# Kernel optimization log

Hardware: AMD Instinct MI355X
Metric: run time of the kernel (lower is better)

## Reference

```python
import jax, jax.numpy as jnp
import numpy as np

K = 16  # K_neighbors

def linear_positions(pixels):
    # normalized flat (pixels, 2) grid positions, matching LinearPositions(normalize=True, flat_output=True)
    wd = int(round(pixels ** 0.5))
    h = jnp.repeat(jnp.arange(wd, dtype=jnp.float32)[:, None], wd, axis=1)
    w = jnp.repeat(jnp.arange(wd, dtype=jnp.float32)[None, :], wd, axis=0)
    pos = jnp.stack([h, w], axis=-1) / (wd - 1)
    return pos.reshape(pixels, 2)


def setup_inputs() -> dict:
    key = jax.random.key(0)
    ks = jax.random.split(key, 8)
    B, Wn, P, C = 4, 16, 256, 32
    inp = {
        "x": jax.random.normal(ks[0], (B, Wn, P, C), dtype=jnp.float32),
        "sf_w0": jax.random.normal(ks[1], (3 * K, 128), dtype=jnp.float32) * 0.05,
        "sf_b0": jnp.zeros((128,), jnp.float32),
        "sf_w1": jax.random.normal(ks[2], (128, 128), dtype=jnp.float32) * 0.05,
        "sf_b1": jnp.zeros((128,), jnp.float32),
        "sf_wo": jax.random.normal(ks[3], (128, 64), dtype=jnp.float32) * 0.05,
        "sf_bo": jnp.zeros((64,), jnp.float32),
        "out_w0": jax.random.normal(ks[4], (C + 64, 128), dtype=jnp.float32) * 0.05,
        "out_b0": jnp.zeros((128,), jnp.float32),
        "out_w1": jax.random.normal(ks[5], (128, 128), dtype=jnp.float32) * 0.05,
        "out_b1": jnp.zeros((128,), jnp.float32),
        "out_wo": jax.random.normal(ks[6], (128, 64), dtype=jnp.float32) * 0.05,
        "out_bo": jnp.zeros((64,), jnp.float32),
    }
    return inp


def reference(x, sf_w0, sf_b0, sf_w1, sf_b1, sf_wo, sf_bo,
              out_w0, out_b0, out_w1, out_b1, out_wo, out_bo):
    B, Wn, P, C = x.shape
    # L1 similarity: 1 - mean |x_i - x_j| over channels -> (B, Wn, P, P)
    w = 1.0 - jnp.mean(jnp.abs(x[:, :, :, None, :] - x[:, :, None, :, :]), axis=-1)
    K_scores, K_idxs = jax.lax.top_k(w, K)  # (B, Wn, P, K)
    pos = linear_positions(P)  # (P, 2)
    # source pos for pixel i minus gathered target pos of its K neighbors
    rel = pos[None, None, :, None, :] - pos[K_idxs]  # (B, Wn, P, K, 2)
    K_rel_pos = rel.reshape(B, Wn, P, K * 2)
    # sf FFN
    h = jnp.concatenate([K_scores, K_rel_pos], axis=-1)  # (B, Wn, P, 3K)
    h = jax.nn.relu(h @ sf_w0 + sf_b0)
    h = jax.nn.relu(h @ sf_w1 + sf_b1)
    sf = h @ sf_wo + sf_bo  # (B, Wn, P, 64)
    # out FFN
    h = jnp.concatenate([x, sf], axis=-1)  # (B, Wn, P, C+64)
    h = jax.nn.relu(h @ out_w0 + out_b0)
    h = jax.nn.relu(h @ out_w1 + out_b1)
    return h @ out_wo + out_bo  # (B, Wn, P, 64)
```

## Files before the change

### kernel.cpp

```cpp
#include <hip/hip_runtime.h>
#include <hip/hip_bf16.h>

#define K_SEL 16
#define NCAND 20

typedef __attribute__((ext_vector_type(8))) short short8;
typedef __attribute__((ext_vector_type(4))) short short4v;
typedef __attribute__((ext_vector_type(4))) float f32x4;

__device__ __forceinline__ short f2bf_bits(float v) {
    union { __hip_bfloat16 b; short s; } u;
    u.b = __float2bfloat16(v);
    return u.s;
}
__device__ __forceinline__ float bf2f_bits(short h) {
    return __uint_as_float(((unsigned)(unsigned short)h) << 16);
}
__device__ __forceinline__ float readlane_f(float v, int l) {
    return __int_as_float(__builtin_amdgcn_readlane(__float_as_int(v), l));
}

__device__ __noinline__ void pack_body(
    int t,
    const float* __restrict__ s0w, const float* __restrict__ s1w,
    const float* __restrict__ sow, const float* __restrict__ o0w,
    const float* __restrict__ o1w, const float* __restrict__ oow,
    short* __restrict__ wpack)
{
    if (t >= 69632) return;
    int l, base;
    if      (t <  8192) { l = 0; base = 0;     }
    else if (t < 24576) { l = 1; base = 8192;  }
    else if (t < 32768) { l = 2; base = 24576; }
    else if (t < 45056) { l = 3; base = 32768; }
    else if (t < 61440) { l = 4; base = 45056; }
    else                { l = 5; base = 61440; }

    const float* W = (l == 0) ? s0w : (l == 1) ? s1w : (l == 2) ? sow
                   : (l == 3) ? o0w : (l == 4) ? o1w : oow;
    int N    = (l == 2 || l == 5) ? 64 : 128;
    int Kr   = (l == 0) ? 48 : (l == 3) ? 96 : 128;
    int woff = (l == 0) ? 0 : (l == 1) ? 16384 : (l == 2) ? 49152
             : (l == 3) ? 65536 : (l == 4) ? 90112 : 122880;
    int sz   = (l == 2 || l == 5) ? 8192 : (l == 3) ? 12288 : (l == 0) ? 8192 : 16384;

    int e = t - base;
    int i = e & 7, kb = (e >> 3) & 3, rem = e >> 5;
    int n = rem % N, ks = rem / N;
    int k = ks * 32 + kb * 8 + i;
    float v = (k < Kr) ? W[k * N + n] : 0.0f;
    short hi = f2bf_bits(v);
    float lo = v - bf2f_bits(hi);
    wpack[woff + e]      = hi;
    wpack[woff + sz + e] = f2bf_bits(lo);
}

template<int COMP>
__device__ __forceinline__ void simtopk_body(
    const float* __restrict__ x, float* __restrict__ feat,
    float* xsT, int* candj, double* rs, int win, int grp, int tid)
{
    const int lane = tid & 63;
    const int wv   = tid >> 6;

    if (tid < 512) {
        const int c4 = tid & 7, jb = tid >> 3;
        const float4* gx = reinterpret_cast<const float4*>(x + (size_t)win * 8192);
        float4 v0 = gx[jb * 8 + c4];
        float4 v1 = gx[jb * 8 + c4 + 512];
        float4 v2 = gx[jb * 8 + c4 + 1024];
        float4 v3 = gx[jb * 8 + c4 + 1536];
        float4* xsT4 = reinterpret_cast<float4*>(xsT);
        const int gsw = jb ^ c4;
        xsT4[(4 * c4 + 0) * 64 + gsw] = make_float4(v0.x, v1.x, v2.x, v3.x);
        xsT4[(4 * c4 + 1) * 64 + gsw] = make_float4(v0.y, v1.y, v2.y, v3.y);
        xsT4[(4 * c4 + 2) * 64 + gsw] = make_float4(v0.z, v1.z, v2.z, v3.z);
        xsT4[(4 * c4 + 3) * 64 + gsw] = make_float4(v0.w, v1.w, v2.w, v3.w);
    }
    __syncthreads();

    const int plbase = (grp & 1) * 32 + wv * 2;

    const f32x4* xsT4c = reinterpret_cast<const f32x4*>(xsT);
    float acc0[4] = {0.f, 0.f, 0.f, 0.f};
    float acc1[4] = {0.f, 0.f, 0.f, 0.f};
    #pragma unroll
    for (int c = 0; c < 32; ++c) {
        f32x4 a = xsT4c[c * 64 + (lane ^ ((c >> 2) & 7))];
        float xi0 = readlane_f(a[COMP], plbase);
        float xi1 = readlane_f(a[COMP], plbase + 1);
        #pragma unroll
        for (int q = 0; q < 4; ++q) {
            acc0[q] += fabsf(a[q] - xi0);
            acc1[q] += fabsf(a[q] - xi1);
        }
    }
    unsigned int p0[4], p1[4];
    #pragma unroll
    for (int q = 0; q < 4; ++q) {
        p0[q] = (__float_as_uint(acc0[q]) & 0xFFFFFF00u) | (unsigned)(q * 64 + lane);
        p1[q] = (__float_as_uint(acc1[q]) & 0xFFFFFF00u) | (unsigned)(q * 64 + lane);
    }

    unsigned int T0 = 0, T1 = 0;
    for (int bit = 31; bit >= 0; --bit) {
        unsigned int c0 = T0 | (1u << bit), c1 = T1 | (1u << bit);
        int n0 = __popcll(__ballot(p0[0] < c0)) + __popcll(__ballot(p0[1] < c0))
               + __popcll(__ballot(p0[2] < c0)) + __popcll(__ballot(p0[3] < c0));
        int n1 = __popcll(__ballot(p1[0] < c1)) + __popcll(__ballot(p1[1] < c1))
               + __popcll(__ballot(p1[2] < c1)) + __popcll(__ballot(p1[3] < c1));
        if (n0 < NCAND) T0 = c0;
        if (n1 < NCAND) T1 = c1;
    }

    const unsigned long long lt = (1ull << lane) - 1ull;
    int base0 = 0, base1 = 0;
    #pragma unroll
    for (int q = 0; q < 4; ++q) {
        bool s0 = (p0[q] <= T0);
        unsigned long long m0 = __ballot(s0);
        if (s0) candj[(wv * 2 + 0) * NCAND + base0 + __popcll(m0 & lt)] = q * 64 + lane;
        base0 += __popcll(m0);
        bool s1 = (p1[q] <= T1);
        unsigned long long m1 = __ballot(s1);
        if (s1) candj[(wv * 2 + 1) * NCAND + base1 + __popcll(m1 & lt)] = q * 64 + lane;
        base1 += __popcll(m1);
    }
    asm volatile("s_waitcnt lgkmcnt(0)" ::: "memory");

    const int t  = lane >> 5;
    const int cl = lane & 31;
    double s = 0.0;
    int myj = -1;
    if (cl < NCAND) {
        myj = candj[(wv * 2 + t) * NCAND + cl];
        const int pwin = COMP * 64 + plbase + t;
        const float4* xj = reinterpret_cast<const float4*>(x + (size_t)win * 8192 + (size_t)myj * 32);
        const float4* xp = reinterpret_cast<const float4*>(x + (size_t)win * 8192 + (size_t)pwin * 32);
        #pragma unroll
        for (int c4 = 0; c4 < 8; ++c4) {
            float4 b = xj[c4];
            float4 a = xp[c4];
            s += fabs((double)a.x - (double)b.x);
            s += fabs((double)a.y - (double)b.y);
            s += fabs((double)a.z - (double)b.z);
            s += fabs((double)a.w - (double)b.w);
        }
        rs[(wv * 2 + t) * NCAND + cl] = s;
    }
    asm volatile("s_waitcnt lgkmcnt(0)" ::: "memory");

    if (cl < NCAND) {
        int rank = 0;
        #pragma unroll 4
        for (int o = 0; o < NCAND; ++o) {
            double so = rs[(wv * 2 + t) * NCAND + o];
            int    jo = candj[(wv * 2 + t) * NCAND + o];
            rank += (so < s || (so == s && jo < myj)) ? 1 : 0;
        }
        if (rank < K_SEL) {
            const int pwin = COMP * 64 + plbase + t;
            const int gp   = win * 256 + pwin;
            feat[gp * 48 + rank] = (float)(1.0 - s * 0.03125);
            float dh = (float)((pwin >> 4) - (myj >> 4)) * (1.0f / 15.0f);
            float dw = (float)((pwin & 15) - (myj & 15)) * (1.0f / 15.0f);
            reinterpret_cast<float2*>(feat)[gp * 24 + 8 + rank] = make_float2(dh, dw);
        }
    }
}

__global__ __launch_bounds__(1024) void simtopk_kernel(
    const float* __restrict__ x,
    float* __restrict__ feat,
    const float* __restrict__ s0w, const float* __restrict__ s1w,
    const float* __restrict__ sow, const float* __restrict__ o0w,
    const float* __restrict__ o1w, const float* __restrict__ oow,
    short* __restrict__ wpack)
{
    __shared__ __align__(16) float xsT[8192];
    __shared__ int    candj[16 * 2 * NCAND];
    __shared__ double rs[16 * 2 * NCAND];

    const int tid = threadIdx.x;

    if (blockIdx.x >= 512) {
        pack_body((blockIdx.x - 512) * 1024 + tid,
                  s0w, s1w, sow, o0w, o1w, oow, wpack);
        return;
    }

    const int win = blockIdx.x >> 3;
    const int grp = blockIdx.x & 7;

    switch (grp >> 1) {
        case 0: simtopk_body<0>(x, feat, xsT, candj, rs, win, grp, tid); break;
        case 1: simtopk_body<1>(x, feat, xsT, candj, rs, win, grp, tid); break;
        case 2: simtopk_body<2>(x, feat, xsT, candj, rs, win, grp, tid); break;
        default: simtopk_body<3>(x, feat, xsT, candj, rs, win, grp, tid); break;
    }
}

template<int K_STEPS, int N, bool RELU, bool TO_GLOBAL>
__device__ __forceinline__ void bf16_layer(
    const short* hiIn, const short* loIn, short* hiOut, short* loOut,
    float* gout, int pbase, const short* __restrict__ wpack, int woff, int sz,
    const float* __restrict__ bias, int wv, int lane, int out_col_off)
{
    if (N == 64 && wv >= 8) return;
    const int mt  = wv & 1;
    const int nt  = wv >> 1;
    const int m_a = mt * 16 + (lane & 15);
    const int kb  = lane >> 4;
    const int n   = nt * 16 + (lane & 15);

    f32x4 acc = (f32x4){0.f, 0.f, 0.f, 0.f};
    #pragma unroll
    for (int ks = 0; ks < K_STEPS; ++ks) {
        const int g   = ks * 4 + kb;
        const int off = m_a * 256 + ((g ^ (m_a & 7)) << 4);
        short8 ahi = *(const short8*)((const char*)hiIn + off);
        short8 alo = *(const short8*)((const char*)loIn + off);
        const int wi = woff + ((ks * N + n) * 4 + kb) * 8;
        short8 whi = *(const short8*)(wpack + wi);
        short8 wlo = *(const short8*)(wpack + wi + sz);
        acc = __builtin_amdgcn_mfma_f32_16x16x32_bf16(ahi, whi, acc, 0, 0, 0);
        acc = __builtin_amdgcn_mfma_f32_16x16x32_bf16(ahi, wlo, acc, 0, 0, 0);
        acc = __builtin_amdgcn_mfma_f32_16x16x32_bf16(alo, whi, acc, 0, 0, 0);
    }

    const float bv = bias[n];
    #pragma unroll
    for (int r = 0; r < 4; ++r) {
        float v = acc[r] + bv;
        if (RELU) v = fmaxf(v, 0.0f);
        const int pw = mt * 16 + (lane >> 4) * 4 + r;
        if (TO_GLOBAL) {
            gout[(size_t)(pbase + pw) * 64 + n] = v;
        } else {
            const int w   = out_col_off + n;
            const int off = pw * 256 + ((((w >> 3) ^ (pw & 7))) << 4) + (w & 7) * 2;
            short h = f2bf_bits(v);
            short l = f2bf_bits(v - bf2f_bits(h));
            *(short*)((char*)hiOut + off) = h;
            *(short*)((char*)loOut + off) = l;
        }
    }
}

__global__ __launch_bounds__(1024) void ffn_kernel(
    const float* __restrict__ x,
    const float* __restrict__ feat,
    const short* __restrict__ wpack,
    const float* __restrict__ s0b, const float* __restrict__ s1b,
    const float* __restrict__ sob, const float* __restrict__ o0b,
    const float* __restrict__ o1b, const float* __restrict__ oob,
    float* __restrict__ out)
{
    __shared__ __align__(16) short hiA[32 * 128];
    __shared__ __align__(16) short loA[32 * 128];
    __shared__ __align__(16) short hiB[32 * 128];
    __shared__ __align__(16) short loB[32 * 128];

    const int tid   = threadIdx.x;
    const int lane  = tid & 63;
    const int wv    = tid >> 6;
    const int pbase = blockIdx.x * 32;

    if (tid < 384) {
        int p = tid / 12, c4 = tid - p * 12;
        f32x4 v = ((const f32x4*)feat)[(size_t)(pbase + p) * 12 + c4];
        short4v h4, l4;
        #pragma unroll
        for (int j = 0; j < 4; ++j) {
            short h = f2bf_bits(v[j]);
            h4[j] = h;
            l4[j] = f2bf_bits(v[j] - bf2f_bits(h));
        }
        int off = p * 256 + ((((c4 >> 1) ^ (p & 7))) << 4) + (c4 & 1) * 8;
        *(short4v*)((char*)hiA + off) = h4;
        *(short4v*)((char*)loA + off) = l4;
    } else if (tid < 512) {
        int t2 = tid - 384;
        int p = t2 & 31, sel = t2 >> 5;
        int g = 6 + (sel & 1);
        int off = p * 256 + ((g ^ (p & 7)) << 4);
        short8 z = (short8){0,0,0,0,0,0,0,0};
        if (sel >> 1) *(short8*)((char*)loA + off) = z;
        else          *(short8*)((char*)hiA + off) = z;
    }
    __syncthreads();

    bf16_layer<2, 128, true, false>(hiA, loA, hiB, loB, nullptr, pbase,
                                    wpack, 0, 8192, s0b, wv, lane, 0);
    __syncthreads();
    bf16_layer<4, 128, true, false>(hiB, loB, hiA, loA, nullptr, pbase,
                                    wpack, 16384, 16384, s1b, wv, lane, 0);
    __syncthreads();
    if (tid < 256) {
        int p = tid >> 3, c4 = tid & 7;
        f32x4 v = ((const f32x4*)x)[(size_t)(pbase + p) * 8 + c4];
        short4v h4, l4;
        #pragma unroll
        for (int j = 0; j < 4; ++j) {
            short h = f2bf_bits(v[j]);
            h4[j] = h;
            l4[j] = f2bf_bits(v[j] - bf2f_bits(h));
        }
        int off = p * 256 + ((((c4 >> 1) ^ (p & 7))) << 4) + (c4 & 1) * 8;
        *(short4v*)((char*)hiB + off) = h4;
        *(short4v*)((char*)loB + off) = l4;
    }
    bf16_layer<4, 64, false, false>(hiA, loA, hiB, loB, nullptr, pbase,
                                    wpack, 49152, 8192, sob, wv, lane, 32);
    __syncthreads();
    bf16_layer<3, 128, true, false>(hiB, loB, hiA, loA, nullptr, pbase,
                                    wpack, 65536, 12288, o0b, wv, lane, 0);
    __syncthreads();
    bf16_layer<4, 128, true, false>(hiA, loA, hiB, loB, nullptr, pbase,
                                    wpack, 90112, 16384, o1b, wv, lane, 0);
    __syncthreads();
    bf16_layer<4, 64, false, true>(hiB, loB, nullptr, nullptr, out, pbase,
                                   wpack, 122880, 8192, oob, wv, lane, 0);
}

extern "C" void kernel_launch(void* const* d_in, const int* in_sizes, int n_in,
                              void* d_out, int out_size, void* d_ws, size_t ws_size,
                              hipStream_t stream) {
    const float* x    = (const float*)d_in[0];
    const float* s0w  = (const float*)d_in[1];
    const float* s0b  = (const float*)d_in[2];
    const float* s1w  = (const float*)d_in[3];
    const float* s1b  = (const float*)d_in[4];
    const float* sow  = (const float*)d_in[5];
    const float* sob  = (const float*)d_in[6];
    const float* o0w  = (const float*)d_in[7];
    const float* o0b  = (const float*)d_in[8];
    const float* o1w  = (const float*)d_in[9];
    const float* o1b  = (const float*)d_in[10];
    const float* oow  = (const float*)d_in[11];
    const float* oob  = (const float*)d_in[12];

    short* wpack = (short*)d_ws;
    float* feat  = (float*)((char*)d_ws + 524288);
    float* out   = (float*)d_out;

    simtopk_kernel<<<580, 1024, 0, stream>>>(x, feat,
                                             s0w, s1w, sow, o0w, o1w, oow, wpack);
    ffn_kernel<<<512, 1024, 0, stream>>>(x, feat, wpack,
                                         s0b, s1b, sob, o0b, o1b, oob,
                                         out);
}
```

Baseline: 53.73 us.

## Process 64 pixels per FFN block with 8 waves reusing weight fragments across M tiles

The FFN kernel now handles 64 pixels per block with 512 threads instead of 32 pixels with 1024 threads. Each wave owns one N tile and loops over several M tiles, so each weight fragment loaded from global memory feeds up to four row tiles instead of one. This cuts global weight traffic per pixel and halves the block count. In exchange it doubles shared memory per block and raises register pressure from the multiple accumulators, and the grid shrinks to 256 blocks, which may leave compute units idle.

```diff
diff --git a/kernel.cpp b/kernel.cpp
--- a/kernel.cpp
+++ b/kernel.cpp
@@ -201,53 +201,62 @@
 }
 
 template<int K_STEPS, int N, bool RELU, bool TO_GLOBAL>
-__device__ __forceinline__ void bf16_layer(
+__device__ __forceinline__ void bf16_layer64(
     const short* hiIn, const short* loIn, short* hiOut, short* loOut,
     float* gout, int pbase, const short* __restrict__ wpack, int woff, int sz,
     const float* __restrict__ bias, int wv, int lane, int out_col_off)
 {
-    if (N == 64 && wv >= 8) return;
-    const int mt  = wv & 1;
-    const int nt  = wv >> 1;
-    const int m_a = mt * 16 + (lane & 15);
-    const int kb  = lane >> 4;
-    const int n   = nt * 16 + (lane & 15);
-
-    f32x4 acc = (f32x4){0.f, 0.f, 0.f, 0.f};
+    const int nt   = (N == 128) ? wv : (wv & 3);
+    const int mt0  = (N == 128) ? 0  : ((wv >> 2) * 2);
+    const int MREP = (N == 128) ? 4  : 2;
+    const int kb   = lane >> 4;
+    const int n    = nt * 16 + (lane & 15);
+
+    f32x4 acc[4];
+    #pragma unroll
+    for (int m = 0; m < 4; ++m) acc[m] = (f32x4){0.f, 0.f, 0.f, 0.f};
+
     #pragma unroll
     for (int ks = 0; ks < K_STEPS; ++ks) {
-        const int g   = ks * 4 + kb;
-        const int off = m_a * 256 + ((g ^ (m_a & 7)) << 4);
-        short8 ahi = *(const short8*)((const char*)hiIn + off);
-        short8 alo = *(const short8*)((const char*)loIn + off);
         const int wi = woff + ((ks * N + n) * 4 + kb) * 8;
         short8 whi = *(const short8*)(wpack + wi);
         short8 wlo = *(const short8*)(wpack + wi + sz);
-        acc = __builtin_amdgcn_mfma_f32_16x16x32_bf16(ahi, whi, acc, 0, 0, 0);
-        acc = __builtin_amdgcn_mfma_f32_16x16x32_bf16(ahi, wlo, acc, 0, 0, 0);
-        acc = __builtin_amdgcn_mfma_f32_16x16x32_bf16(alo, whi, acc, 0, 0, 0);
+        const int g = ks * 4 + kb;
+        #pragma unroll
+        for (int m = 0; m < MREP; ++m) {
+            const int m_a = (mt0 + m) * 16 + (lane & 15);
+            const int off = m_a * 256 + ((g ^ (m_a & 7)) << 4);
+            short8 ahi = *(const short8*)((const char*)hiIn + off);
+            short8 alo = *(const short8*)((const char*)loIn + off);
+            acc[m] = __builtin_amdgcn_mfma_f32_16x16x32_bf16(ahi, whi, acc[m], 0, 0, 0);
+            acc[m] = __builtin_amdgcn_mfma_f32_16x16x32_bf16(ahi, wlo, acc[m], 0, 0, 0);
+            acc[m] = __builtin_amdgcn_mfma_f32_16x16x32_bf16(alo, whi, acc[m], 0, 0, 0);
+        }
     }
 
     const float bv = bias[n];
     #pragma unroll
-    for (int r = 0; r < 4; ++r) {
-        float v = acc[r] + bv;
-        if (RELU) v = fmaxf(v, 0.0f);
-        const int pw = mt * 16 + (lane >> 4) * 4 + r;
-        if (TO_GLOBAL) {
-            gout[(size_t)(pbase + pw) * 64 + n] = v;
-        } else {
-            const int w   = out_col_off + n;
-            const int off = pw * 256 + ((((w >> 3) ^ (pw & 7))) << 4) + (w & 7) * 2;
-            short h = f2bf_bits(v);
-            short l = f2bf_bits(v - bf2f_bits(h));
-            *(short*)((char*)hiOut + off) = h;
-            *(short*)((char*)loOut + off) = l;
-        }
-    }
-}
-
-__global__ __launch_bounds__(1024) void ffn_kernel(
+    for (int m = 0; m < MREP; ++m) {
+        #pragma unroll
+        for (int r = 0; r < 4; ++r) {
+            float v = acc[m][r] + bv;
+            if (RELU) v = fmaxf(v, 0.0f);
+            const int pw = (mt0 + m) * 16 + (lane >> 4) * 4 + r;
+            if (TO_GLOBAL) {
+                gout[(size_t)(pbase + pw) * 64 + n] = v;
+            } else {
+                const int w   = out_col_off + n;
+                const int off = pw * 256 + ((((w >> 3) ^ (pw & 7))) << 4) + (w & 7) * 2;
+                short h = f2bf_bits(v);
+                short l = f2bf_bits(v - bf2f_bits(h));
+                *(short*)((char*)hiOut + off) = h;
+                *(short*)((char*)loOut + off) = l;
+            }
+        }
+    }
+}
+
+__global__ __launch_bounds__(512) void ffn_kernel(
     const float* __restrict__ x,
     const float* __restrict__ feat,
     const short* __restrict__ wpack,
@@ -256,32 +265,36 @@
     const float* __restrict__ o1b, const float* __restrict__ oob,
     float* __restrict__ out)
 {
-    __shared__ __align__(16) short hiA[32 * 128];
-    __shared__ __align__(16) short loA[32 * 128];
-    __shared__ __align__(16) short hiB[32 * 128];
-    __shared__ __align__(16) short loB[32 * 128];
+    __shared__ __align__(16) short hiA[64 * 128];
+    __shared__ __align__(16) short loA[64 * 128];
+    __shared__ __align__(16) short hiB[64 * 128];
+    __shared__ __align__(16) short loB[64 * 128];
 
     const int tid   = threadIdx.x;
     const int lane  = tid & 63;
     const int wv    = tid >> 6;
-    const int pbase = blockIdx.x * 32;
-
-    if (tid < 384) {
-        int p = tid / 12, c4 = tid - p * 12;
-        f32x4 v = ((const f32x4*)feat)[(size_t)(pbase + p) * 12 + c4];
-        short4v h4, l4;
-        #pragma unroll
-        for (int j = 0; j < 4; ++j) {
-            short h = f2bf_bits(v[j]);
-            h4[j] = h;
-            l4[j] = f2bf_bits(v[j] - bf2f_bits(h));
-        }
-        int off = p * 256 + ((((c4 >> 1) ^ (p & 7))) << 4) + (c4 & 1) * 8;
-        *(short4v*)((char*)hiA + off) = h4;
-        *(short4v*)((char*)loA + off) = l4;
-    } else if (tid < 512) {
-        int t2 = tid - 384;
-        int p = t2 & 31, sel = t2 >> 5;
+    const int pbase = blockIdx.x * 64;
+
+    #pragma unroll
+    for (int rr = 0; rr < 2; ++rr) {
+        int u = tid + rr * 512;
+        if (u < 768) {
+            int p = u / 12, c4 = u - p * 12;
+            f32x4 v = ((const f32x4*)feat)[(size_t)(pbase + p) * 12 + c4];
+            short4v h4, l4;
+            #pragma unroll
+            for (int j = 0; j < 4; ++j) {
+                short h = f2bf_bits(v[j]);
+                h4[j] = h;
+                l4[j] = f2bf_bits(v[j] - bf2f_bits(h));
+            }
+            int off = p * 256 + ((((c4 >> 1) ^ (p & 7))) << 4) + (c4 & 1) * 8;
+            *(short4v*)((char*)hiA + off) = h4;
+            *(short4v*)((char*)loA + off) = l4;
+        }
+    }
+    if (tid < 256) {
+        int p = tid >> 2, sel = tid & 3;
         int g = 6 + (sel & 1);
         int off = p * 256 + ((g ^ (p & 7)) << 4);
         short8 z = (short8){0,0,0,0,0,0,0,0};
@@ -290,13 +303,13 @@
     }
     __syncthreads();
 
-    bf16_layer<2, 128, true, false>(hiA, loA, hiB, loB, nullptr, pbase,
-                                    wpack, 0, 8192, s0b, wv, lane, 0);
-    __syncthreads();
-    bf16_layer<4, 128, true, false>(hiB, loB, hiA, loA, nullptr, pbase,
-                                    wpack, 16384, 16384, s1b, wv, lane, 0);
-    __syncthreads();
-    if (tid < 256) {
+    bf16_layer64<2, 128, true, false>(hiA, loA, hiB, loB, nullptr, pbase,
+                                      wpack, 0, 8192, s0b, wv, lane, 0);
+    __syncthreads();
+    bf16_layer64<4, 128, true, false>(hiB, loB, hiA, loA, nullptr, pbase,
+                                      wpack, 16384, 16384, s1b, wv, lane, 0);
+    __syncthreads();
+    {
         int p = tid >> 3, c4 = tid & 7;
         f32x4 v = ((const f32x4*)x)[(size_t)(pbase + p) * 8 + c4];
         short4v h4, l4;
@@ -310,17 +323,17 @@
         *(short4v*)((char*)hiB + off) = h4;
         *(short4v*)((char*)loB + off) = l4;
     }
-    bf16_layer<4, 64, false, false>(hiA, loA, hiB, loB, nullptr, pbase,
-                                    wpack, 49152, 8192, sob, wv, lane, 32);
-    __syncthreads();
-    bf16_layer<3, 128, true, false>(hiB, loB, hiA, loA, nullptr, pbase,
-                                    wpack, 65536, 12288, o0b, wv, lane, 0);
-    __syncthreads();
-    bf16_layer<4, 128, true, false>(hiA, loA, hiB, loB, nullptr, pbase,
-                                    wpack, 90112, 16384, o1b, wv, lane, 0);
-    __syncthreads();
-    bf16_layer<4, 64, false, true>(hiB, loB, nullptr, nullptr, out, pbase,
-                                   wpack, 122880, 8192, oob, wv, lane, 0);
+    bf16_layer64<4, 64, false, false>(hiA, loA, hiB, loB, nullptr, pbase,
+                                      wpack, 49152, 8192, sob, wv, lane, 32);
+    __syncthreads();
+    bf16_layer64<3, 128, true, false>(hiB, loB, hiA, loA, nullptr, pbase,
+                                      wpack, 65536, 12288, o0b, wv, lane, 0);
+    __syncthreads();
+    bf16_layer64<4, 128, true, false>(hiA, loA, hiB, loB, nullptr, pbase,
+                                      wpack, 90112, 16384, o1b, wv, lane, 0);
+    __syncthreads();
+    bf16_layer64<4, 64, false, true>(hiB, loB, nullptr, nullptr, out, pbase,
+                                     wpack, 122880, 8192, oob, wv, lane, 0);
 }
 
 extern "C" void kernel_launch(void* const* d_in, const int* in_sizes, int n_in,
@@ -346,7 +359,7 @@
 
     simtopk_kernel<<<580, 1024, 0, stream>>>(x, feat,
                                              s0w, s1w, sow, o0w, o1w, oow, wpack);
-    ffn_kernel<<<512, 1024, 0, stream>>>(x, feat, wpack,
-                                         s0b, s1b, sob, o0b, o1b, oob,
-                                         out);
-}
+    ffn_kernel<<<256, 512, 0, stream>>>(x, feat, wpack,
+                                        s0b, s1b, sob, o0b, o1b, oob,
+                                        out);
+}
```

Measured after the change: 50.00 us (median of 2 runs). 1.07x faster.
